# Optimization experiments

Measured on AMD Instinct MI355X. Metric: run time of the kernel, lower is better.

The kernel has to match this reference:

```python
import jax, jax.numpy as jnp
import numpy as np

N_PARTICLES = 10_000_000
GRID_N = 256  # per-axis grid size
GRID_EDGE = 10.0  # grid spans [-10, 10] in each axis


def setup_inputs() -> dict:
    key = jax.random.key(0)
    k1, k2 = jax.random.split(key)
    # uniform in [-11, 11]: some particles fall outside the grid -> exercises bounds mask
    positions = jax.random.uniform(k1, (N_PARTICLES, 3), dtype=jnp.float32,
                                   minval=-11.0, maxval=11.0)
    weights = jax.random.uniform(k2, (N_PARTICLES,), dtype=jnp.float32)
    return {"positions": positions, "weights": weights}


def reference(positions, weights):
    # Grid buffers (from Grid.__init__ with grid_edges=(10,10,10), n=(256,256,256))
    n = GRID_N
    grid_min = jnp.full((3,), -GRID_EDGE, dtype=positions.dtype)
    grid_max = jnp.full((3,), GRID_EDGE, dtype=positions.dtype)
    dx = (grid_max - grid_min) / (n - 1)  # [3]

    # float index: fi = (pos - min)/dx  -> nearest grid point via trunc(fi + 0.5)
    fi = (positions - grid_min[None, :]) / dx[None, :]          # [N,3]
    i = (fi + 0.5).astype(jnp.int32)  # C-style trunc-toward-zero, matches torch .type(int64)

    gd = jnp.all((i >= 0) & (i < n), axis=1)                    # [N] in-grid mask

    # flatten 3D index; out-of-grid particles routed to index 0 with zero weight
    flat = (i[:, 0] * n + i[:, 1]) * n + i[:, 2]                # [N]
    flat = jnp.where(gd, flat, 0)
    w = jnp.where(gd, weights, jnp.zeros_like(weights))

    grid = jnp.zeros((n * n * n,), dtype=positions.dtype).at[flat].add(w)
    return grid.reshape(n, n, n)
```

## Files before the change

### kernel.cpp

```cpp
#include <hip/hip_runtime.h>
#include <stdint.h>


constexpr int GRID_N = 256;
constexpr int SB     = 1024;
constexpr int CELLS  = 16384;
constexpr int NB     = 256;
constexpr int BT     = 1024;
constexpr int RING   = 16;
constexpr int RSTR   = 17;
constexpr uint32_t SIDE_CAP = 65536;

__device__ __forceinline__ int particle_flat(float px, float py, float pz) {
#pragma clang fp contract(off)
    float fix = (px + 10.0f) * 12.75f;
    float fiy = (py + 10.0f) * 12.75f;
    float fiz = (pz + 10.0f) * 12.75f;
    int ix = (int)(fix + 0.5f);
    int iy = (int)(fiy + 0.5f);
    int iz = (int)(fiz + 0.5f);
    bool in = (ix >= 0) & (ix < GRID_N) &
              (iy >= 0) & (iy < GRID_N) &
              (iz >= 0) & (iz < GRID_N);
    return in ? ((ix << 16) | (iy << 8) | iz) : -1;
}

__global__ __launch_bounds__(1024) void k0_init(uint32_t* __restrict__ gcur,
                                                uint32_t* __restrict__ side_n,
                                                uint32_t C)
{
    int t = blockIdx.x * blockDim.x + threadIdx.x;
    if (t < SB) gcur[t] = (uint32_t)t * C;
    if (t == 0) *side_n = 0;
}

__global__ __launch_bounds__(BT, 1) void k3_direct(
    const float* __restrict__ pos, const float* __restrict__ wgt,
    uint32_t* __restrict__ gcur, uint2* __restrict__ pairs,
    uint2* __restrict__ side, uint32_t* __restrict__ side_n,
    uint32_t C, int n)
{
    __shared__ uint2    stg[SB][RSTR];
    __shared__ uint32_t s_total[SB];
    __shared__ uint32_t s_flushed[SB];
    __shared__ uint32_t s_wl[SB];
    __shared__ uint32_t s_wldst[SB];
    __shared__ uint32_t s_wln;

    const int tid = threadIdx.x;
    const int blk = blockIdx.x;

    s_total[tid]   = 0;
    s_flushed[tid] = 0;
    if (tid == 0) s_wln = 0;
    __syncthreads();

    const float4* p4 = (const float4*)pos;
    const float4* w4 = (const float4*)wgt;
    int ngroups = n >> 2;
    int G = NB * BT;
    int iters = (ngroups + G - 1) / G;

    for (int it = 0; it < iters; ++it) {
        if (tid == 0) s_wln = 0;
        int g = blk * BT + tid + it * G;
        if (g < ngroups) {
            float4 a = p4[(size_t)g * 3 + 0];
            float4 b = p4[(size_t)g * 3 + 1];
            float4 c = p4[(size_t)g * 3 + 2];
            float4 w = w4[g];
            int   f[4]  = { particle_flat(a.x, a.y, a.z), particle_flat(a.w, b.x, b.y),
                            particle_flat(b.z, b.w, c.x), particle_flat(c.y, c.z, c.w) };
            float ww[4] = { w.x, w.y, w.z, w.w };
#pragma unroll
            for (int k = 0; k < 4; ++k) {
                int fk = f[k];
                if (fk >= 0) {
                    uint32_t bin  = (uint32_t)fk >> 14;
                    uint32_t slot = atomicAdd(&s_total[bin], 1u);
                    if (slot - s_flushed[bin] < (uint32_t)RING) {
                        stg[bin][slot & (RING - 1)] =
                            make_uint2((uint32_t)fk & (CELLS - 1), __float_as_uint(ww[k]));
                    } else {
                        atomicSub(&s_total[bin], 1u);
                        uint32_t si = atomicAdd(side_n, 1u);
                        if (si < SIDE_CAP)
                            side[si] = make_uint2((uint32_t)fk, __float_as_uint(ww[k]));
                    }
                }
            }
        }
        __syncthreads();
        {
            uint32_t p = s_total[tid] - s_flushed[tid];
            if (p >= 8u) {
                uint32_t o   = s_flushed[tid];
                uint32_t dst = atomicAdd(&gcur[tid], 8u);
                if (dst + 8u <= (uint32_t)(tid + 1) * C) {
                    uint32_t wi = atomicAdd(&s_wln, 1u);
                    s_wl[wi]    = ((uint32_t)tid << 4) | (o & (RING - 1));
                    s_wldst[wi] = dst;
                } else {
                    atomicSub(&gcur[tid], 8u);
                    for (int j = 0; j < 8; ++j) {
                        uint2 v = stg[tid][(o + j) & (RING - 1)];
                        uint32_t si = atomicAdd(side_n, 1u);
                        if (si < SIDE_CAP)
                            side[si] = make_uint2(((uint32_t)tid << 14) | v.x, v.y);
                    }
                }
                s_flushed[tid] = o + 8u;
            }
        }
        __syncthreads();
        {
            uint32_t m = s_wln;
            for (uint32_t j = tid; j < m * 8u; j += BT) {
                uint32_t e = s_wl[j >> 3];
                uint2 v = stg[e >> 4][((e & (RING - 1)) + (j & 7u)) & (RING - 1)];
                uint64_t v64 = (uint64_t)v.x | ((uint64_t)v.y << 32);
                __builtin_nontemporal_store(v64,
                    (uint64_t*)&pairs[(size_t)s_wldst[j >> 3] + (j & 7u)]);
            }
        }
        __syncthreads();
    }

    if (blk == 0 && tid == 0) {
        for (int p = n & ~3; p < n; ++p) {
            int f = particle_flat(pos[3 * p], pos[3 * p + 1], pos[3 * p + 2]);
            if (f >= 0) {
                uint32_t si = atomicAdd(side_n, 1u);
                if (si < SIDE_CAP)
                    side[si] = make_uint2((uint32_t)f, __float_as_uint(wgt[p]));
            }
        }
    }

    {
        uint32_t t = s_total[tid];
        uint32_t p = t - s_flushed[tid];
        uint32_t pad = ((p + 7u) & ~7u) - p;
        for (uint32_t j = 0; j < pad; ++j)
            stg[tid][(t + j) & (RING - 1)] = make_uint2(0u, 0u);
        s_total[tid] = t + pad;
    }
    __syncthreads();

    for (int r = 0; r < 2; ++r) {
        if (tid == 0) s_wln = 0;
        __syncthreads();
        {
            uint32_t p = s_total[tid] - s_flushed[tid];
            if (p >= 8u) {
                uint32_t o   = s_flushed[tid];
                uint32_t dst = atomicAdd(&gcur[tid], 8u);
                if (dst + 8u <= (uint32_t)(tid + 1) * C) {
                    uint32_t wi = atomicAdd(&s_wln, 1u);
                    s_wl[wi]    = ((uint32_t)tid << 4) | (o & (RING - 1));
                    s_wldst[wi] = dst;
                } else {
                    atomicSub(&gcur[tid], 8u);
                    for (int j = 0; j < 8; ++j) {
                        uint2 v = stg[tid][(o + j) & (RING - 1)];
                        uint32_t si = atomicAdd(side_n, 1u);
                        if (si < SIDE_CAP)
                            side[si] = make_uint2(((uint32_t)tid << 14) | v.x, v.y);
                    }
                }
                s_flushed[tid] = o + 8u;
            }
        }
        __syncthreads();
        {
            uint32_t m = s_wln;
            for (uint32_t j = tid; j < m * 8u; j += BT) {
                uint32_t e = s_wl[j >> 3];
                uint2 v = stg[e >> 4][((e & (RING - 1)) + (j & 7u)) & (RING - 1)];
                uint64_t v64 = (uint64_t)v.x | ((uint64_t)v.y << 32);
                __builtin_nontemporal_store(v64,
                    (uint64_t*)&pairs[(size_t)s_wldst[j >> 3] + (j & 7u)]);
            }
        }
        __syncthreads();
    }
}

__global__ __launch_bounds__(BT) void k4_direct(const uint2* __restrict__ pairs,
                                                const uint32_t* __restrict__ gcur,
                                                const uint2* __restrict__ side,
                                                const uint32_t* __restrict__ side_n,
                                                uint32_t C,
                                                float* __restrict__ grid)
{
    __shared__ float acc[CELLS];
    for (int i = threadIdx.x; i < CELLS; i += BT) acc[i] = 0.0f;
    __syncthreads();

    int b = blockIdx.x;
    uint32_t s = (uint32_t)b * C, e = gcur[b];
    for (uint32_t i = s + threadIdx.x; i < e; i += BT) {
        uint2 p = pairs[i];
        atomicAdd(&acc[p.x], __uint_as_float(p.y));
    }
    uint32_t ns = *side_n;
    if (ns > SIDE_CAP) ns = SIDE_CAP;
    for (uint32_t i = threadIdx.x; i < ns; i += BT) {
        uint2 sv = side[i];
        if ((int)(sv.x >> 14) == b)
            atomicAdd(&acc[sv.x & (CELLS - 1)], __uint_as_float(sv.y));
    }
    __syncthreads();

    float4* out4 = (float4*)(grid + (size_t)b * CELLS);
    const float4* a4 = (const float4*)acc;
    for (int i = threadIdx.x; i < CELLS / 4; i += BT) out4[i] = a4[i];
}

__global__ __launch_bounds__(BT) void k1_hist(const float* __restrict__ pos,
                                              uint32_t* __restrict__ hist,
                                              int n)
{
    __shared__ uint32_t h[SB];
    for (int i = threadIdx.x; i < SB; i += BT) h[i] = 0;
    __syncthreads();

    const float4* p4 = (const float4*)pos;
    int ngroups = n >> 2;
    int G = gridDim.x * BT;
    for (int g = blockIdx.x * BT + threadIdx.x; g < ngroups; g += G) {
        float4 a = p4[(size_t)g * 3 + 0];
        float4 b = p4[(size_t)g * 3 + 1];
        float4 c = p4[(size_t)g * 3 + 2];
        int f0 = particle_flat(a.x, a.y, a.z);
        int f1 = particle_flat(a.w, b.x, b.y);
        int f2 = particle_flat(b.z, b.w, c.x);
        int f3 = particle_flat(c.y, c.z, c.w);
        if (f0 >= 0) atomicAdd(&h[f0 >> 14], 1u);
        if (f1 >= 0) atomicAdd(&h[f1 >> 14], 1u);
        if (f2 >= 0) atomicAdd(&h[f2 >> 14], 1u);
        if (f3 >= 0) atomicAdd(&h[f3 >> 14], 1u);
    }
    if (blockIdx.x == 0 && threadIdx.x == 0) {
        for (int p = n & ~3; p < n; ++p) {
            int f = particle_flat(pos[3 * p], pos[3 * p + 1], pos[3 * p + 2]);
            if (f >= 0) atomicAdd(&h[f >> 14], 1u);
        }
    }
    __syncthreads();
    uint32_t* out = hist + (size_t)blockIdx.x * SB;
    for (int i = threadIdx.x; i < SB; i += BT) out[i] = h[i];
}

__global__ __launch_bounds__(128) void k2a_colscan(const uint32_t* __restrict__ hist,
                                                   uint32_t* __restrict__ offs,
                                                   uint32_t* __restrict__ totals)
{
    int b = blockIdx.x * 128 + threadIdx.x;
    uint32_t run = 0;
    for (int blk = 0; blk < NB; blk += 8) {
        uint32_t v[8];
#pragma unroll
        for (int j = 0; j < 8; ++j)
            v[j] = hist[(size_t)(blk + j) * SB + b];
#pragma unroll
        for (int j = 0; j < 8; ++j) {
            offs[(size_t)(blk + j) * SB + b] = run;
            run += v[j];
        }
    }
    totals[b] = run;
}

__global__ __launch_bounds__(256) void k2b_scan(const uint32_t* __restrict__ totals,
                                                uint32_t* __restrict__ base)
{
    __shared__ uint32_t part[256];
    int t = threadIdx.x;
    uint32_t local[4];
    uint32_t s = 0;
#pragma unroll
    for (int j = 0; j < 4; ++j) { local[j] = totals[t * 4 + j]; s += local[j]; }
    part[t] = s;
    __syncthreads();
    if (t == 0) {
        uint32_t run = 0;
        for (int i = 0; i < 256; ++i) { uint32_t tmp = part[i]; part[i] = run; run += tmp; }
    }
    __syncthreads();
    uint32_t run = part[t];
#pragma unroll
    for (int j = 0; j < 4; ++j) { base[t * 4 + j] = run; run += local[j]; }
    if (t == 255) base[SB] = run;
}

__global__ __launch_bounds__(BT) void k3_scatter(const float* __restrict__ pos,
                                                 const float* __restrict__ wgt,
                                                 const uint32_t* __restrict__ offs,
                                                 const uint32_t* __restrict__ base,
                                                 uint2* __restrict__ pairs,
                                                 int n)
{
    __shared__ uint32_t cur[SB];
    for (int i = threadIdx.x; i < SB; i += BT)
        cur[i] = base[i] + offs[(size_t)blockIdx.x * SB + i];
    __syncthreads();

    const float4* p4 = (const float4*)pos;
    const float4* w4 = (const float4*)wgt;
    int ngroups = n >> 2;
    int G = gridDim.x * BT;
    for (int g = blockIdx.x * BT + threadIdx.x; g < ngroups; g += G) {
        float4 a = p4[(size_t)g * 3 + 0];
        float4 b = p4[(size_t)g * 3 + 1];
        float4 c = p4[(size_t)g * 3 + 2];
        float4 w = w4[g];
        int   f[4]  = { particle_flat(a.x, a.y, a.z), particle_flat(a.w, b.x, b.y),
                        particle_flat(b.z, b.w, c.x), particle_flat(c.y, c.z, c.w) };
        float ww[4] = { w.x, w.y, w.z, w.w };
#pragma unroll
        for (int k = 0; k < 4; ++k) {
            if (f[k] >= 0) {
                uint32_t slot = atomicAdd(&cur[f[k] >> 14], 1u);
                pairs[slot] = make_uint2((uint32_t)(f[k] & (CELLS - 1)),
                                         __float_as_uint(ww[k]));
            }
        }
    }
    if (blockIdx.x == 0 && threadIdx.x == 0) {
        for (int p = n & ~3; p < n; ++p) {
            int f = particle_flat(pos[3 * p], pos[3 * p + 1], pos[3 * p + 2]);
            if (f >= 0) {
                uint32_t slot = atomicAdd(&cur[f >> 14], 1u);
                pairs[slot] = make_uint2((uint32_t)(f & (CELLS - 1)),
                                         __float_as_uint(wgt[p]));
            }
        }
    }
}

__global__ __launch_bounds__(BT) void k4_seg(const uint2* __restrict__ pairs,
                                             const uint32_t* __restrict__ base,
                                             float* __restrict__ grid)
{
    __shared__ float acc[CELLS];
    for (int i = threadIdx.x; i < CELLS; i += BT) acc[i] = 0.0f;
    __syncthreads();

    int b = blockIdx.x;
    uint32_t s = base[b], e = base[b + 1];
    for (uint32_t i = s + threadIdx.x; i < e; i += BT) {
        uint2 p = pairs[i];
        atomicAdd(&acc[p.x], __uint_as_float(p.y));
    }
    __syncthreads();

    float4* out4 = (float4*)(grid + (size_t)b * CELLS);
    const float4* a4 = (const float4*)acc;
    for (int i = threadIdx.x; i < CELLS / 4; i += BT) out4[i] = a4[i];
}

__global__ __launch_bounds__(256) void forcegrid_scatter_atomic(
    const float* __restrict__ pos, const float* __restrict__ wgt,
    float* __restrict__ grid, int n)
{
    int t = blockIdx.x * blockDim.x + threadIdx.x;
    long long bse = (long long)t * 4;
    if (bse >= n) return;
    const float4* p4 = (const float4*)pos;
    float4 a = p4[(size_t)t * 3 + 0];
    float4 b = p4[(size_t)t * 3 + 1];
    float4 c = p4[(size_t)t * 3 + 2];
    float4 w = ((const float4*)wgt)[t];
    int   f[4]  = { particle_flat(a.x, a.y, a.z), particle_flat(a.w, b.x, b.y),
                    particle_flat(b.z, b.w, c.x), particle_flat(c.y, c.z, c.w) };
    float ww[4] = { w.x, w.y, w.z, w.w };
#pragma unroll
    for (int k = 0; k < 4; ++k) {
        if (bse + k >= n) break;
        if (f[k] >= 0) atomicAdd(&grid[f[k]], ww[k]);
    }
}

extern "C" void kernel_launch(void* const* d_in, const int* in_sizes, int n_in,
                              void* d_out, int out_size, void* d_ws, size_t ws_size,
                              hipStream_t stream)
{
    const float* pos = (const float*)d_in[0];
    const float* wgt = (const float*)d_in[1];
    float* grid = (float*)d_out;
    int n = in_sizes[0] / 3;

    uint32_t C = ((2u * (uint32_t)(n / SB) + 4096u) + 7u) & ~7u;
    if (C < 1024u) C = 1024u;
    size_t o1 = 0;
    uint2*    pairs1 = (uint2*)d_ws;                     o1 += (size_t)SB * C * sizeof(uint2);
    uint2*    side   = (uint2*)((char*)d_ws + o1);       o1 += (size_t)SIDE_CAP * sizeof(uint2);
    uint32_t* gcur   = (uint32_t*)((char*)d_ws + o1);    o1 += (size_t)SB * 4;
    uint32_t* side_n = (uint32_t*)((char*)d_ws + o1);    o1 += 64;

    if (ws_size >= o1) {
        k0_init  <<<1,  1024, 0, stream>>>(gcur, side_n, C);
        k3_direct<<<NB, BT,   0, stream>>>(pos, wgt, gcur, pairs1, side, side_n, C, n);
        k4_direct<<<SB, BT,   0, stream>>>(pairs1, gcur, side, side_n, C, grid);
        return;
    }

    size_t o2 = 0;
    uint2*    pairs2  = (uint2*)d_ws;                    o2 += (size_t)n * sizeof(uint2);
    uint32_t* hist2   = (uint32_t*)((char*)d_ws + o2);   o2 += (size_t)NB * SB * 4;
    uint32_t* offs2   = (uint32_t*)((char*)d_ws + o2);   o2 += (size_t)NB * SB * 4;
    uint32_t* totals2 = (uint32_t*)((char*)d_ws + o2);   o2 += (size_t)SB * 4;
    uint32_t* base2   = (uint32_t*)((char*)d_ws + o2);   o2 += (size_t)(SB + 1) * 4;

    if (ws_size >= o2) {
        k1_hist    <<<NB,       BT,  0, stream>>>(pos, hist2, n);
        k2a_colscan<<<SB / 128, 128, 0, stream>>>(hist2, offs2, totals2);
        k2b_scan   <<<1,        256, 0, stream>>>(totals2, base2);
        k3_scatter <<<NB,       BT,  0, stream>>>(pos, wgt, offs2, base2, pairs2, n);
        k4_seg     <<<SB,       BT,  0, stream>>>(pairs2, base2, grid);
    } else {
        hipMemsetAsync(grid, 0, (size_t)out_size * sizeof(float), stream);
        int groups = (n + 3) / 4;
        forcegrid_scatter_atomic<<<(groups + 255) / 256, 256, 0, stream>>>(pos, wgt, grid, n);
    }
}
```

Before: 295.5 us.

## Prefetch next particle batch in bin kernel and vectorize segment accumulation loads

The binning kernel now loads the next iteration's positions and weights into registers before processing the current batch, so global load latency overlaps with the shared-memory binning and flush phases. Barriers are replaced by an LDS-only waitcnt plus s_barrier, so the in-flight prefetch loads are not drained at each barrier. The direct accumulation kernel reads pairs two at a time with 128-bit nontemporal loads and writes the grid with nontemporal stores. The costs are higher register pressure, and the vectorized pair loop assumes 16-byte aligned segments of even length, which relies on segment starts being multiples of 8 and the padding done earlier.

Result: no change. 297.7 us (+0.7%).

```diff
diff --git a/kernel.cpp b/kernel.cpp
--- a/kernel.cpp
+++ b/kernel.cpp
@@ -10,6 +10,14 @@
 constexpr int RING   = 16;
 constexpr int RSTR   = 17;
 constexpr uint32_t SIDE_CAP = 65536;
+
+typedef unsigned int u32x4 __attribute__((ext_vector_type(4)));
+typedef float        f32x4 __attribute__((ext_vector_type(4)));
+
+#define BAR_LGKM() do { \
+    asm volatile("s_waitcnt lgkmcnt(0)" ::: "memory"); \
+    __builtin_amdgcn_s_barrier(); \
+} while (0)
 
 __device__ __forceinline__ int particle_flat(float px, float py, float pz) {
 #pragma clang fp contract(off)
@@ -61,14 +69,30 @@
     int G = NB * BT;
     int iters = (ngroups + G - 1) / G;
 
+    int g = blk * BT + tid;
+    bool valid = g < ngroups;
+    float4 a = {}, b = {}, c = {}, w = {};
+    if (valid) {
+        a = p4[(size_t)g * 3 + 0];
+        b = p4[(size_t)g * 3 + 1];
+        c = p4[(size_t)g * 3 + 2];
+        w = w4[g];
+    }
+
     for (int it = 0; it < iters; ++it) {
         if (tid == 0) s_wln = 0;
-        int g = blk * BT + tid + it * G;
-        if (g < ngroups) {
-            float4 a = p4[(size_t)g * 3 + 0];
-            float4 b = p4[(size_t)g * 3 + 1];
-            float4 c = p4[(size_t)g * 3 + 2];
-            float4 w = w4[g];
+
+        int gn = g + G;
+        bool v2 = (it + 1 < iters) && (gn < ngroups);
+        float4 a2 = {}, b2 = {}, c2 = {}, w2 = {};
+        if (v2) {
+            a2 = p4[(size_t)gn * 3 + 0];
+            b2 = p4[(size_t)gn * 3 + 1];
+            c2 = p4[(size_t)gn * 3 + 2];
+            w2 = w4[gn];
+        }
+
+        if (valid) {
             int   f[4]  = { particle_flat(a.x, a.y, a.z), particle_flat(a.w, b.x, b.y),
                             particle_flat(b.z, b.w, c.x), particle_flat(c.y, c.z, c.w) };
             float ww[4] = { w.x, w.y, w.z, w.w };
@@ -90,7 +114,7 @@
                 }
             }
         }
-        __syncthreads();
+        BAR_LGKM();
         {
             uint32_t p = s_total[tid] - s_flushed[tid];
             if (p >= 8u) {
@@ -112,7 +136,7 @@
                 s_flushed[tid] = o + 8u;
             }
         }
-        __syncthreads();
+        BAR_LGKM();
         {
             uint32_t m = s_wln;
             for (uint32_t j = tid; j < m * 8u; j += BT) {
@@ -123,7 +147,9 @@
                     (uint64_t*)&pairs[(size_t)s_wldst[j >> 3] + (j & 7u)]);
             }
         }
-        __syncthreads();
+        BAR_LGKM();
+
+        a = a2; b = b2; c = c2; w = w2; valid = v2; g = gn;
     }
 
     if (blk == 0 && tid == 0) {
@@ -199,9 +225,12 @@
 
     int b = blockIdx.x;
     uint32_t s = (uint32_t)b * C, e = gcur[b];
-    for (uint32_t i = s + threadIdx.x; i < e; i += BT) {
-        uint2 p = pairs[i];
-        atomicAdd(&acc[p.x], __uint_as_float(p.y));
+    const u32x4* pp = (const u32x4*)(pairs + s);
+    uint32_t m = (e - s) >> 1;
+    for (uint32_t i = threadIdx.x; i < m; i += BT) {
+        u32x4 v = __builtin_nontemporal_load(&pp[i]);
+        atomicAdd(&acc[v.x], __uint_as_float(v.y));
+        atomicAdd(&acc[v.z], __uint_as_float(v.w));
     }
     uint32_t ns = *side_n;
     if (ns > SIDE_CAP) ns = SIDE_CAP;
@@ -212,9 +241,10 @@
     }
     __syncthreads();
 
-    float4* out4 = (float4*)(grid + (size_t)b * CELLS);
-    const float4* a4 = (const float4*)acc;
-    for (int i = threadIdx.x; i < CELLS / 4; i += BT) out4[i] = a4[i];
+    f32x4* out4 = (f32x4*)(grid + (size_t)b * CELLS);
+    const f32x4* a4 = (const f32x4*)acc;
+    for (int i = threadIdx.x; i < CELLS / 4; i += BT)
+        __builtin_nontemporal_store(a4[i], &out4[i]);
 }
 
 __global__ __launch_bounds__(BT) void k1_hist(const float* __restrict__ pos,
@@ -420,7 +450,7 @@
         k3_scatter <<<NB,       BT,  0, stream>>>(pos, wgt, offs2, base2, pairs2, n);
         k4_seg     <<<SB,       BT,  0, stream>>>(pairs2, base2, grid);
     } else {
-        hipMemsetAsync(grid, 0, (size_t)out_size * sizeof(float), stream);
+        (void)hipMemsetAsync(grid, 0, (size_t)out_size * sizeof(float), stream);
         int groups = (n + 3) / 4;
         forcegrid_scatter_atomic<<<(groups + 255) / 256, 256, 0, stream>>>(pos, wgt, grid, n);
     }
```
